# Kernel optimization log

Hardware: AMD Instinct MI355X
Metric: run time of the kernel (lower is better)

Reference implementation:

```python
import jax, jax.numpy as jnp
import numpy as np

P_BINS = 5
T_BINS = 16
B_BINS = P_BINS * T_BINS  # 80
IN_CH = 16
OUT_CH = 32
N_VERTS = 30000   # mesh vertices (cols of conn)
N_PATCH = 30000   # patches (rows of conn / B)
K_NNZ = 3         # nnz per sparse row (interpolation support)


def setup_inputs() -> dict:
    key = jax.random.key(0)
    k1, k2, k3, k4 = jax.random.split(key, 4)
    x = jax.random.normal(k1, (N_VERTS, IN_CH), dtype=jnp.float32)
    conn_idx = jax.random.randint(k2, (N_PATCH * B_BINS, K_NNZ), 0, N_VERTS, dtype=jnp.int32)
    conn_val = jax.random.uniform(k3, (N_PATCH * B_BINS, K_NNZ), dtype=jnp.float32)
    weights = jax.random.normal(k4, (B_BINS, IN_CH, OUT_CH), dtype=jnp.float32)
    return {"x": x, "conn_idx": conn_idx, "conn_val": conn_val, "weights": weights}


def _rotated_weights(weights):
    # layer_weights[j, :, :, i] = weights[(j + p*i) % B]  -> reshape (B*inp, out*t)
    j = jnp.arange(B_BINS)[:, None]
    i = jnp.arange(T_BINS)[None, :]
    idx = (j + P_BINS * i) % B_BINS                       # (B, t)
    lw = weights[idx]                                     # (B, t, inp, out)
    lw = jnp.transpose(lw, (0, 2, 3, 1))                  # (B, inp, out, t)
    return lw.reshape(B_BINS * IN_CH, OUT_CH * T_BINS)


def reference(x, conn_idx, conn_val, weights):
    # sparse.mm(conn, x): gather K vertex features per bin row and weight-sum
    gathered = jnp.einsum('rk,rkc->rc', conn_val, x[conn_idx])  # (N*B, inp)
    h = gathered.reshape(-1, B_BINS * IN_CH)                    # (N, B*inp)
    lw = _rotated_weights(weights)                              # (B*inp, out*t)
    y = h @ lw                                                  # (N, out*t)
    y = y.reshape(-1, OUT_CH, T_BINS)
    return jnp.max(y, axis=-1)                                  # (N, out)
```

## Files before the change

### kernel.cpp

```cpp
#include <hip/hip_runtime.h>
#include <hip/hip_bf16.h>
#include <stdint.h>

#define NP 30000
#define BBINS 80
#define INCH 16
#define OUTCH 32
#define KDIM 1280
#define NDIM 512
#define KSTEPS 40
#define NROWS (NP * BBINS)

typedef __bf16 bf16x8 __attribute__((ext_vector_type(8)));
typedef __bf16 bf16x4 __attribute__((ext_vector_type(4)));
typedef float f32x4 __attribute__((ext_vector_type(4)));

__device__ __forceinline__ void async_ld16(const void* g, void* l) {
    __builtin_amdgcn_global_load_lds(
        (const __attribute__((address_space(1))) unsigned int*)g,
        (__attribute__((address_space(3))) unsigned int*)l,
        16, 0, 0);
}

__global__ void prep_weights(const float* __restrict__ w, __bf16* __restrict__ pw) {
    int gid = blockIdx.x * 256 + threadIdx.x;
    int e  = gid & 7;
    int qs = (gid >> 3) & 3;
    int n  = (gid >> 5) & 511;
    int kc = gid >> 14;
    int kp = kc * 32 + ((qs ^ (n & 3)) << 3) + e;
    int b = kp >> 4, c = kp & 15;
    int o = n >> 4,  t = n & 15;
    int bid = (b + 5 * t) % BBINS;
    pw[gid] = (__bf16)w[(bid * INCH + c) * OUTCH + o];
}

__global__ __launch_bounds__(256) void gather_h(
    const float* __restrict__ x,
    const int*   __restrict__ cidx,
    const float* __restrict__ cval,
    __bf16* __restrict__ h) {
    const int gid = blockIdx.x * 256 + threadIdx.x;
    const int r = gid >> 2;
    const int q = gid & 3;
    const int r3 = r * 3;
    const int i0 = cidx[r3 + 0], i1 = cidx[r3 + 1], i2 = cidx[r3 + 2];
    const float v0 = cval[r3 + 0], v1 = cval[r3 + 1], v2 = cval[r3 + 2];
    const float4 a = *(const float4*)(x + (size_t)i0 * 16 + q * 4);
    const float4 b = *(const float4*)(x + (size_t)i1 * 16 + q * 4);
    const float4 c = *(const float4*)(x + (size_t)i2 * 16 + q * 4);
    bf16x4 hv;
    hv[0] = (__bf16)(v0 * a.x + v1 * b.x + v2 * c.x);
    hv[1] = (__bf16)(v0 * a.y + v1 * b.y + v2 * c.y);
    hv[2] = (__bf16)(v0 * a.z + v1 * b.z + v2 * c.z);
    hv[3] = (__bf16)(v0 * a.w + v1 * b.w + v2 * c.w);
    *(bf16x4*)((char*)h + (size_t)gid * 8) = hv;
}

__global__ __launch_bounds__(256, 2) void gemm_max(
    const __bf16* __restrict__ h,
    const __bf16* __restrict__ pw,
    float* __restrict__ out) {

    __shared__ __align__(16) __bf16 Alds[128 * 32];
    __shared__ __align__(16) __bf16 Blds[256 * 32];

    const int bid = blockIdx.x;
    const int m    = (bid >> 4) * 8 + (bid & 7);
    const int ncol = (bid >> 3) & 1;
    if (m >= 235) return;
    const int mbase = m * 128;

    const int tid  = threadIdx.x;
    const int lane = tid & 63;
    const int wave = tid >> 6;
    const int wave_mrow = wave >> 1;
    const int wave_ncol = wave & 1;

    int a_off[4], b_off[8];
    {
        const int ml = lane & 15, q = lane >> 4;
#pragma unroll
        for (int i = 0; i < 4; ++i)
            a_off[i] = (wave_mrow * 64 + i * 16 + ml) * 64 + q * 16;
#pragma unroll
        for (int j = 0; j < 8; ++j) {
            int nl = wave_ncol * 128 + j * 16 + ml;
            b_off[j] = nl * 64 + ((q ^ (nl & 3)) << 4);
        }
    }

    f32x4 acc[4][8];
#pragma unroll
    for (int i = 0; i < 4; ++i)
#pragma unroll
        for (int j = 0; j < 8; ++j)
            acc[i][j] = (f32x4){0.f, 0.f, 0.f, 0.f};

    const char* hB  = (const char*)h;
    const char* pwB = (const char*)pw + ncol * 16384 + tid * 16;
    int rg0 = mbase + (tid >> 2);
    int rg1 = rg0 + 64;
    if (rg0 > NP - 1) rg0 = NP - 1;
    if (rg1 > NP - 1) rg1 = NP - 1;
    const char* aSrc0 = hB + (size_t)rg0 * 2560 + (tid & 3) * 16;
    const char* aSrc1 = hB + (size_t)rg1 * 2560 + (tid & 3) * 16;
    char* aDst0 = (char*)Alds + tid * 16;
    char* aDst1 = aDst0 + 4096;
    char* bDst  = (char*)Blds + tid * 16;

    for (int kc = 0; kc < KSTEPS; ++kc) {
        const char* bs = pwB + kc * 32768;
#pragma unroll
        for (int i = 0; i < 4; ++i)
            async_ld16(bs + i * 4096, bDst + i * 4096);
        async_ld16(aSrc0 + kc * 64, aDst0);
        async_ld16(aSrc1 + kc * 64, aDst1);
        __syncthreads();

        bf16x8 af[4], bfr[8];
#pragma unroll
        for (int i = 0; i < 4; ++i)
            af[i] = *(const bf16x8*)((const char*)Alds + a_off[i]);
#pragma unroll
        for (int j = 0; j < 8; ++j)
            bfr[j] = *(const bf16x8*)((const char*)Blds + b_off[j]);
#pragma unroll
        for (int i = 0; i < 4; ++i)
#pragma unroll
            for (int j = 0; j < 8; ++j)
                acc[i][j] = __builtin_amdgcn_mfma_f32_16x16x32_bf16(
                    af[i], bfr[j], acc[i][j], 0, 0, 0);
        __syncthreads();
    }

    const int rgrp = lane >> 4;
    const int tl   = lane & 15;
#pragma unroll
    for (int i = 0; i < 4; ++i) {
#pragma unroll
        for (int j = 0; j < 8; ++j) {
            float v0 = acc[i][j][0], v1 = acc[i][j][1];
            float v2 = acc[i][j][2], v3 = acc[i][j][3];
#pragma unroll
            for (int off = 1; off < 16; off <<= 1) {
                v0 = fmaxf(v0, __shfl_xor(v0, off));
                v1 = fmaxf(v1, __shfl_xor(v1, off));
                v2 = fmaxf(v2, __shfl_xor(v2, off));
                v3 = fmaxf(v3, __shfl_xor(v3, off));
            }
            if (tl == 0) {
                const int o  = ncol * 16 + wave_ncol * 8 + j;
                const int pr = mbase + wave_mrow * 64 + i * 16 + rgrp * 4;
                if (pr + 0 < NP) out[(pr + 0) * 32 + o] = v0;
                if (pr + 1 < NP) out[(pr + 1) * 32 + o] = v1;
                if (pr + 2 < NP) out[(pr + 2) * 32 + o] = v2;
                if (pr + 3 < NP) out[(pr + 3) * 32 + o] = v3;
            }
        }
    }
}

extern "C" void kernel_launch(void* const* d_in, const int* in_sizes, int n_in,
                              void* d_out, int out_size, void* d_ws, size_t ws_size,
                              hipStream_t stream) {
    const float* x    = (const float*)d_in[0];
    const int*   cidx = (const int*)d_in[1];
    const float* cval = (const float*)d_in[2];
    const float* w    = (const float*)d_in[3];
    float* out = (float*)d_out;

    __bf16* pw = (__bf16*)d_ws;
    __bf16* h  = (__bf16*)((char*)d_ws + (2 << 20));

    hipLaunchKernelGGL(prep_weights, dim3(2560), dim3(256), 0, stream, w, pw);
    hipLaunchKernelGGL(gather_h, dim3(NROWS * 4 / 256), dim3(256), 0, stream,
                       x, cidx, cval, h);
    hipLaunchKernelGGL(gemm_max, dim3(480), dim3(256), 0, stream,
                       h, (const __bf16*)pw, out);
}
```

Before: 189.4 us.

## Double-buffer GEMM LDS loads, swizzle A/B layouts, batch gather rows per thread

The GEMM now stages the next K-chunk into a second LDS buffer while computing on the current one, which replaces the two full barriers per step with a single wait and barrier. A and B tiles get a new XOR swizzle based on (row>>1)&3, applied in both the weight prep and the A load addresses, to reduce LDS bank conflicts. The gather kernel processes four rows per thread with strided indexing so more independent loads are in flight, and it launches a quarter of the threads. Doubling LDS use may lower occupancy.

After: 202.1 us. +6.7%, slower.

```diff
diff --git a/kernel.cpp b/kernel.cpp
--- a/kernel.cpp
+++ b/kernel.cpp
@@ -10,6 +10,8 @@
 #define NDIM 512
 #define KSTEPS 40
 #define NROWS (NP * BBINS)
+#define RPT 4
+#define RSTRIDE (NROWS / RPT)
 
 typedef __bf16 bf16x8 __attribute__((ext_vector_type(8)));
 typedef __bf16 bf16x4 __attribute__((ext_vector_type(4)));
@@ -28,7 +30,7 @@
     int qs = (gid >> 3) & 3;
     int n  = (gid >> 5) & 511;
     int kc = gid >> 14;
-    int kp = kc * 32 + ((qs ^ (n & 3)) << 3) + e;
+    int kp = kc * 32 + ((qs ^ ((n >> 1) & 3)) << 3) + e;
     int b = kp >> 4, c = kp & 15;
     int o = n >> 4,  t = n & 15;
     int bid = (b + 5 * t) % BBINS;
@@ -41,20 +43,33 @@
     const float* __restrict__ cval,
     __bf16* __restrict__ h) {
     const int gid = blockIdx.x * 256 + threadIdx.x;
-    const int r = gid >> 2;
-    const int q = gid & 3;
-    const int r3 = r * 3;
-    const int i0 = cidx[r3 + 0], i1 = cidx[r3 + 1], i2 = cidx[r3 + 2];
-    const float v0 = cval[r3 + 0], v1 = cval[r3 + 1], v2 = cval[r3 + 2];
-    const float4 a = *(const float4*)(x + (size_t)i0 * 16 + q * 4);
-    const float4 b = *(const float4*)(x + (size_t)i1 * 16 + q * 4);
-    const float4 c = *(const float4*)(x + (size_t)i2 * 16 + q * 4);
-    bf16x4 hv;
-    hv[0] = (__bf16)(v0 * a.x + v1 * b.x + v2 * c.x);
-    hv[1] = (__bf16)(v0 * a.y + v1 * b.y + v2 * c.y);
-    hv[2] = (__bf16)(v0 * a.z + v1 * b.z + v2 * c.z);
-    hv[3] = (__bf16)(v0 * a.w + v1 * b.w + v2 * c.w);
-    *(bf16x4*)((char*)h + (size_t)gid * 8) = hv;
+    const int rb = gid >> 2;
+    const int q  = gid & 3;
+
+    int   i0[RPT], i1[RPT], i2[RPT];
+    float v0[RPT], v1[RPT], v2[RPT];
+#pragma unroll
+    for (int k = 0; k < RPT; ++k) {
+        const int r3 = (rb + k * RSTRIDE) * 3;
+        i0[k] = cidx[r3 + 0]; i1[k] = cidx[r3 + 1]; i2[k] = cidx[r3 + 2];
+        v0[k] = cval[r3 + 0]; v1[k] = cval[r3 + 1]; v2[k] = cval[r3 + 2];
+    }
+    float4 a[RPT], b[RPT], c[RPT];
+#pragma unroll
+    for (int k = 0; k < RPT; ++k) {
+        a[k] = *(const float4*)(x + (size_t)i0[k] * 16 + q * 4);
+        b[k] = *(const float4*)(x + (size_t)i1[k] * 16 + q * 4);
+        c[k] = *(const float4*)(x + (size_t)i2[k] * 16 + q * 4);
+    }
+#pragma unroll
+    for (int k = 0; k < RPT; ++k) {
+        bf16x4 hv;
+        hv[0] = (__bf16)(v0[k] * a[k].x + v1[k] * b[k].x + v2[k] * c[k].x);
+        hv[1] = (__bf16)(v0[k] * a[k].y + v1[k] * b[k].y + v2[k] * c[k].y);
+        hv[2] = (__bf16)(v0[k] * a[k].z + v1[k] * b[k].z + v2[k] * c[k].z);
+        hv[3] = (__bf16)(v0[k] * a[k].w + v1[k] * b[k].w + v2[k] * c[k].w);
+        *(bf16x4*)((char*)h + (size_t)(rb + k * RSTRIDE) * 32 + q * 8) = hv;
+    }
 }
 
 __global__ __launch_bounds__(256, 2) void gemm_max(
@@ -62,8 +77,8 @@
     const __bf16* __restrict__ pw,
     float* __restrict__ out) {
 
-    __shared__ __align__(16) __bf16 Alds[128 * 32];
-    __shared__ __align__(16) __bf16 Blds[256 * 32];
+    __shared__ __align__(16) __bf16 Alds[2][128 * 32];
+    __shared__ __align__(16) __bf16 Blds[2][256 * 32];
 
     const int bid = blockIdx.x;
     const int m    = (bid >> 4) * 8 + (bid & 7);
@@ -80,13 +95,14 @@
     int a_off[4], b_off[8];
     {
         const int ml = lane & 15, q = lane >> 4;
+        const int f = (ml >> 1) & 3;
 #pragma unroll
         for (int i = 0; i < 4; ++i)
-            a_off[i] = (wave_mrow * 64 + i * 16 + ml) * 64 + q * 16;
+            a_off[i] = (wave_mrow * 64 + i * 16 + ml) * 64 + ((q ^ f) << 4);
 #pragma unroll
         for (int j = 0; j < 8; ++j) {
             int nl = wave_ncol * 128 + j * 16 + ml;
-            b_off[j] = nl * 64 + ((q ^ (nl & 3)) << 4);
+            b_off[j] = nl * 64 + ((q ^ f) << 4);
         }
     }
 
@@ -103,36 +119,54 @@
     int rg1 = rg0 + 64;
     if (rg0 > NP - 1) rg0 = NP - 1;
     if (rg1 > NP - 1) rg1 = NP - 1;
-    const char* aSrc0 = hB + (size_t)rg0 * 2560 + (tid & 3) * 16;
-    const char* aSrc1 = hB + (size_t)rg1 * 2560 + (tid & 3) * 16;
-    char* aDst0 = (char*)Alds + tid * 16;
-    char* aDst1 = aDst0 + 4096;
-    char* bDst  = (char*)Blds + tid * 16;
+    const int swz = ((tid & 3) ^ ((tid >> 3) & 3)) * 16;
+    const char* aSrc0 = hB + (size_t)rg0 * 2560 + swz;
+    const char* aSrc1 = hB + (size_t)rg1 * 2560 + swz;
+    char* aDstB = (char*)Alds + tid * 16;
+    char* bDstB = (char*)Blds + tid * 16;
+
+#define STAGE(kc_, buf_)                                                     \
+    do {                                                                     \
+        const char* bs_ = pwB + (kc_) * 32768;                               \
+        char* bD_ = bDstB + (buf_) * 16384;                                  \
+        char* aD_ = aDstB + (buf_) * 8192;                                   \
+        async_ld16(bs_ + 0 * 4096, bD_ + 0 * 4096);                          \
+        async_ld16(bs_ + 1 * 4096, bD_ + 1 * 4096);                          \
+        async_ld16(bs_ + 2 * 4096, bD_ + 2 * 4096);                          \
+        async_ld16(bs_ + 3 * 4096, bD_ + 3 * 4096);                          \
+        async_ld16(aSrc0 + (kc_) * 64, aD_);                                 \
+        async_ld16(aSrc1 + (kc_) * 64, aD_ + 4096);                          \
+    } while (0)
+
+    STAGE(0, 0);
+    asm volatile("s_waitcnt vmcnt(0)" ::: "memory");
+    __builtin_amdgcn_s_barrier();
 
     for (int kc = 0; kc < KSTEPS; ++kc) {
-        const char* bs = pwB + kc * 32768;
+        const int cur = kc & 1;
+        if (kc + 1 < KSTEPS)
+            STAGE(kc + 1, cur ^ 1);
+
+        const char* A = (const char*)Alds + cur * 8192;
+        const char* B = (const char*)Blds + cur * 16384;
+        bf16x8 af[4], bfr[8];
 #pragma unroll
         for (int i = 0; i < 4; ++i)
-            async_ld16(bs + i * 4096, bDst + i * 4096);
-        async_ld16(aSrc0 + kc * 64, aDst0);
-        async_ld16(aSrc1 + kc * 64, aDst1);
-        __syncthreads();
-
-        bf16x8 af[4], bfr[8];
-#pragma unroll
-        for (int i = 0; i < 4; ++i)
-            af[i] = *(const bf16x8*)((const char*)Alds + a_off[i]);
+            af[i] = *(const bf16x8*)(A + a_off[i]);
 #pragma unroll
         for (int j = 0; j < 8; ++j)
-            bfr[j] = *(const bf16x8*)((const char*)Blds + b_off[j]);
+            bfr[j] = *(const bf16x8*)(B + b_off[j]);
 #pragma unroll
         for (int i = 0; i < 4; ++i)
 #pragma unroll
             for (int j = 0; j < 8; ++j)
                 acc[i][j] = __builtin_amdgcn_mfma_f32_16x16x32_bf16(
                     af[i], bfr[j], acc[i][j], 0, 0, 0);
-        __syncthreads();
-    }
+
+        asm volatile("s_waitcnt vmcnt(0)" ::: "memory");
+        __builtin_amdgcn_s_barrier();
+    }
+#undef STAGE
 
     const int rgrp = lane >> 4;
     const int tl   = lane & 15;
@@ -174,7 +208,7 @@
     __bf16* h  = (__bf16*)((char*)d_ws + (2 << 20));
 
     hipLaunchKernelGGL(prep_weights, dim3(2560), dim3(256), 0, stream, w, pw);
-    hipLaunchKernelGGL(gather_h, dim3(NROWS * 4 / 256), dim3(256), 0, stream,
+    hipLaunchKernelGGL(gather_h, dim3(NROWS / 256), dim3(256), 0, stream,
                        x, cidx, cval, h);
     hipLaunchKernelGGL(gemm_max, dim3(480), dim3(256), 0, stream,
                        h, (const __bf16*)pw, out);
```
